# Kernel tuning notes

Hardware: AMD Instinct MI355X
Metric: run time of the kernel (lower is better)

## Reference

```python
import jax, jax.numpy as jnp
import numpy as np

B, S, H, NH = 2, 2048, 1024, 16
HD = H // NH  # head dim = 64


def setup_inputs() -> dict:
    key = jax.random.key(0)
    k_in, k_q, k_kv, k_o = jax.random.split(key, 4)
    scale = 0.02
    return {
        "inputs": jax.random.normal(k_in, (B, S, H), dtype=jnp.float32),
        "Wq": jax.random.normal(k_q, (H, H), dtype=jnp.float32) * scale,
        "bq": jnp.zeros((H,), dtype=jnp.float32),
        "Wkv": jax.random.normal(k_kv, (H, 2 * H), dtype=jnp.float32) * scale,
        "bkv": jnp.zeros((2 * H,), dtype=jnp.float32),
        "Wo": jax.random.normal(k_o, (H, H), dtype=jnp.float32) * scale,
        "bo": jnp.zeros((H,), dtype=jnp.float32),
    }


def reference(inputs, Wq, bq, Wkv, bkv, Wo, bo):
    b, s, h = inputs.shape
    q = inputs @ Wq + bq                      # [B,S,H]
    kv = inputs @ Wkv + bkv                   # [B,S,2H]
    k, v = kv[..., :h], kv[..., h:]           # each [B,S,H]
    q = q.reshape(b, s, NH, HD)
    k = k.reshape(b, s, NH, HD)
    v = v.reshape(b, s, NH, HD)
    inv_sqrt_d = jnp.asarray(1.0 / np.sqrt(HD), dtype=inputs.dtype)
    scores = jnp.einsum("bqhd,bkhd->bhqk", q, k) * inv_sqrt_d  # [B,NH,S,S]
    probs = jax.nn.softmax(scores, axis=-1)
    attended = jnp.einsum("bhqk,bkhd->bqhd", probs, v)         # [B,S,NH,HD]
    attended = attended.reshape(b, s, h)
    return attended @ Wo + bo
```

## Files before the change

### kernel.cpp

```cpp
#include <hip/hip_runtime.h>
#include <cstdint>

typedef __bf16 bf16;
typedef __attribute__((ext_vector_type(8))) __bf16 bf16x8;
typedef __attribute__((ext_vector_type(4))) __bf16 bf16v4;
typedef __attribute__((ext_vector_type(4))) float f32x4;
typedef __attribute__((ext_vector_type(16))) float f32x16;

#define MFMA16(a, b, c) __builtin_amdgcn_mfma_f32_16x16x32_bf16((a), (b), (c), 0, 0, 0)
#define MFMA32(a, b, c) __builtin_amdgcn_mfma_f32_32x32x16_bf16((a), (b), (c), 0, 0, 0)

#define BATCH 2
#define SLEN 2048
#define HDIM 1024
#define NHEAD 16
#define HEADD 64
#define MROWS (BATCH * SLEN)

#define CEXP 0.1803368801f

typedef __attribute__((address_space(3))) void lds_void;
typedef const __attribute__((address_space(1))) void glb_void;
__device__ __forceinline__ void load_lds16(const bf16* g, bf16* l) {
    __builtin_amdgcn_global_load_lds((glb_void*)g, (lds_void*)l, 16, 0, 0);
}

__global__ __launch_bounds__(256) void prep_kernel(const float* __restrict__ X,
                                                   const float* __restrict__ Wq,
                                                   const float* __restrict__ Wkv,
                                                   const float* __restrict__ Wo,
                                                   const float* __restrict__ bq,
                                                   const float* __restrict__ bkv,
                                                   bf16* __restrict__ Xbf,
                                                   bf16* __restrict__ WqkvT,
                                                   bf16* __restrict__ WoT,
                                                   float* __restrict__ bqkv) {
    const int blk = blockIdx.x;
    const int tid = threadIdx.x;
    if (blk < 4096) {
        int i = (blk * 256 + tid) * 4;
        float4 v = *(const float4*)&X[i];
        bf16v4 o;
        o[0] = (bf16)v.x; o[1] = (bf16)v.y; o[2] = (bf16)v.z; o[3] = (bf16)v.w;
        *(bf16v4*)&Xbf[i] = o;
        return;
    }
    if (blk < 8192) {
        const float* in; bf16* out; int C, id;
        if (blk < 5120)      { in = Wq;  out = WqkvT;                C = 1024; id = blk - 4096; }
        else if (blk < 7168) { in = Wkv; out = WqkvT + 1024 * 1024;  C = 2048; id = blk - 5120; }
        else                 { in = Wo;  out = WoT;                  C = 1024; id = blk - 7168; }
        const int R = 1024;
        const int nbx = C / 32;
        const int j0 = (id % nbx) * 32, i0 = (id / nbx) * 32;
        const int tx = tid & 31, ty = tid >> 5;
        __shared__ float t[32][33];
        for (int r = ty; r < 32; r += 8)
            t[r][tx] = in[(size_t)(i0 + r) * C + j0 + tx];
        __syncthreads();
        for (int r = ty; r < 32; r += 8)
            out[(size_t)(j0 + r) * R + i0 + tx] = (bf16)t[tx][r];
        return;
    }
    int i = (blk - 8192) * 256 + tid;
    if (i < 3072) bqkv[i] = (i < 1024) ? bq[i] : bkv[i - 1024];
}

template <int BM, int BN, int EPI>
__global__ __launch_bounds__(256) void gemm2_kernel(const bf16* __restrict__ A,
                                                    const bf16* __restrict__ BT,
                                                    const float* __restrict__ bias,
                                                    bf16* __restrict__ oQ,
                                                    bf16* __restrict__ oK,
                                                    bf16* __restrict__ oVT,
                                                    float* __restrict__ oF, int K) {
    constexpr int WM = BM / 2, WN = BN / 2;
    constexpr int MT = WM / 16, NT = WN / 16;

    const int tid = threadIdx.x;
    const int lane = tid & 63, wid = tid >> 6;
    const int l15 = lane & 15, quad = lane >> 4;
    const int wm = (wid >> 1) * WM, wn = (wid & 1) * WN;
    const int m0 = blockIdx.y * BM, n0 = blockIdx.x * BN;

    __shared__ bf16 As[BM * 32];
    __shared__ bf16 Bs[BN * 32];

    f32x4 acc[MT][NT] = {};

    const bf16* Ag = A + (size_t)m0 * K;
    const bf16* Bg = BT + (size_t)n0 * K;
    const int arow = lane >> 2, acol = (lane & 3) * 8;

    for (int k0 = 0; k0 < K; k0 += 32) {
#pragma unroll
        for (int t = 0; t < BM / 64; ++t) {
            int tt = t * 4 + wid;
            load_lds16(Ag + (size_t)(tt * 16 + arow) * K + k0 + acol, &As[tt * 512]);
        }
#pragma unroll
        for (int t = 0; t < BN / 64; ++t) {
            int tt = t * 4 + wid;
            load_lds16(Bg + (size_t)(tt * 16 + arow) * K + k0 + acol, &Bs[tt * 512]);
        }
        __syncthreads();

        bf16x8 af[MT], bfr[NT];
#pragma unroll
        for (int i = 0; i < MT; ++i)
            af[i] = *(const bf16x8*)&As[(wm + i * 16 + l15) * 32 + quad * 8];
#pragma unroll
        for (int j = 0; j < NT; ++j)
            bfr[j] = *(const bf16x8*)&Bs[(wn + j * 16 + l15) * 32 + quad * 8];
#pragma unroll
        for (int i = 0; i < MT; ++i)
#pragma unroll
            for (int j = 0; j < NT; ++j)
                acc[i][j] = MFMA16(af[i], bfr[j], acc[i][j]);
        __syncthreads();
    }

#pragma unroll
    for (int i = 0; i < MT; ++i) {
#pragma unroll
        for (int j = 0; j < NT; ++j) {
            const int mb = m0 + wm + i * 16 + quad * 4;
            const int n = n0 + wn + j * 16 + l15;
            const float bv = bias[n];
            if (EPI == 2) {
                float* o = oF + (size_t)mb * 1024 + n;
#pragma unroll
                for (int r = 0; r < 4; ++r) o[(size_t)r * 1024] = acc[i][j][r] + bv;
            } else if (n0 < 1024) {
#pragma unroll
                for (int r = 0; r < 4; ++r)
                    oQ[(size_t)(mb + r) * 1024 + n] = (bf16)((acc[i][j][r] + bv) * CEXP);
            } else if (n0 < 2048) {
#pragma unroll
                for (int r = 0; r < 4; ++r)
                    oK[(size_t)(mb + r) * 1024 + (n - 1024)] = (bf16)(acc[i][j][r] + bv);
            } else {
                const int hd = n - 2048;
                const int bb = mb >> 11, ss = mb & 2047;
                bf16v4 pk;
#pragma unroll
                for (int r = 0; r < 4; ++r) pk[r] = (bf16)(acc[i][j][r] + bv);
                *(bf16v4*)&oVT[((size_t)(bb << 10) + hd) * 2048 + ss] = pk;
            }
        }
    }
}

__global__ __launch_bounds__(256) void attn6_kernel(const bf16* __restrict__ Q,
                                                    const bf16* __restrict__ K,
                                                    const bf16* __restrict__ VT,
                                                    bf16* __restrict__ O) {
    const int bid = blockIdx.x;
    const int xcd = bid & 7, j = bid >> 3;
    const int bh = xcd * 4 + (j >> 4);
    const int q0 = (j & 15) * 128;
    const int b = bh >> 4, head = bh & 15;
    const int tid = threadIdx.x;
    const int lane = tid & 63, wid = tid >> 6;
    const int l31 = lane & 31, hh = lane >> 5;

    __shared__ bf16 Ks[128 * 64];
    __shared__ bf16 VTs[64 * 128];
    __shared__ bf16 Ps[4][32 * 72];

    const int qw = q0 + wid * 32;
    bf16x8 qf[4];
#pragma unroll
    for (int kd = 0; kd < 4; ++kd)
        qf[kd] = *(const bf16x8*)&Q[(size_t)(b * SLEN + qw + l31) * HDIM +
                                    head * 64 + kd * 16 + hh * 8];

    f32x16 o_acc[2] = {};
    float l_lane = 0.f;

    const bf16* Kg = K + (size_t)b * SLEN * HDIM + head * 64;
    const bf16* Vg = VT + (size_t)bh * 64 * SLEN;

    const int r8 = lane >> 3, p8 = lane & 7;
    const int r16 = lane >> 4, p16 = lane & 15;

    for (int kt = 0; kt < 16; ++kt) {
        const int k0 = kt * 128;
#pragma unroll
        for (int pass = 0; pass < 4; ++pass) {
            const int rbk = pass * 32 + wid * 8;
            load_lds16(Kg + (size_t)(k0 + rbk + r8) * HDIM + ((p8 ^ ((rbk + r8) & 7)) * 8),
                       &Ks[rbk * 64]);
            const int rbv = pass * 16 + wid * 4;
            load_lds16(Vg + (size_t)(rbv + r16) * SLEN + k0 + ((p16 ^ ((rbv + r16) & 15)) * 8),
                       &VTs[rbv * 128]);
        }
        __syncthreads();

#pragma unroll
        for (int h = 0; h < 2; ++h) {
            f32x16 sacc[2] = {};
#pragma unroll
            for (int kd = 0; kd < 4; ++kd)
#pragma unroll
                for (int m = 0; m < 2; ++m) {
                    const int key = (h * 2 + m) * 32 + l31;
                    const int c = (kd * 2 + hh) ^ (key & 7);
                    bf16x8 kf = *(const bf16x8*)&Ks[key * 64 + c * 8];
                    sacc[m] = MFMA32(kf, qf[kd], sacc[m]);
                }

#pragma unroll
            for (int m = 0; m < 2; ++m)
#pragma unroll
                for (int g = 0; g < 4; ++g) {
                    bf16v4 pk;
#pragma unroll
                    for (int r = 0; r < 4; ++r) {
                        float p = __builtin_amdgcn_exp2f(sacc[m][g * 4 + r]);
                        l_lane += p;
                        pk[r] = (bf16)p;
                    }
                    *(bf16v4*)&Ps[wid][l31 * 72 + m * 32 + g * 8 + 4 * hh] = pk;
                }

#pragma unroll
            for (int kstep = 0; kstep < 4; ++kstep) {
                bf16x8 pf = *(const bf16x8*)&Ps[wid][l31 * 72 + kstep * 16 + hh * 8];
#pragma unroll
                for (int dt = 0; dt < 2; ++dt) {
                    const int d = dt * 32 + l31;
                    const int cc = ((h * 4 + kstep) * 2 + hh) ^ (d & 15);
                    bf16x8 vf = *(const bf16x8*)&VTs[d * 128 + cc * 8];
                    o_acc[dt] = MFMA32(vf, pf, o_acc[dt]);
                }
            }
        }
        __syncthreads();
    }

    const float l_full = l_lane + __shfl_xor(l_lane, 32, 64);
    const float inv = 1.f / l_full;
    bf16* orow = O + (size_t)(b * SLEN + qw + l31) * HDIM + head * 64;
#pragma unroll
    for (int mt = 0; mt < 2; ++mt)
#pragma unroll
        for (int g = 0; g < 4; ++g) {
            bf16v4 pk;
#pragma unroll
            for (int r = 0; r < 4; ++r) pk[r] = (bf16)(o_acc[mt][g * 4 + r] * inv);
            *(bf16v4*)&orow[mt * 32 + g * 8 + 4 * hh] = pk;
        }
}

extern "C" void kernel_launch(void* const* d_in, const int* in_sizes, int n_in,
                              void* d_out, int out_size, void* d_ws, size_t ws_size,
                              hipStream_t stream) {
    const float* X   = (const float*)d_in[0];
    const float* Wq  = (const float*)d_in[1];
    const float* bq  = (const float*)d_in[2];
    const float* Wkv = (const float*)d_in[3];
    const float* bkv = (const float*)d_in[4];
    const float* Wo  = (const float*)d_in[5];
    const float* bo  = (const float*)d_in[6];
    float* out = (float*)d_out;

    char* ws = (char*)d_ws;
    bf16* Xbf   = (bf16*)(ws);
    bf16* WqkvT = (bf16*)(ws + (8ull << 20));
    bf16* WoT   = (bf16*)(ws + (14ull << 20));
    float* bqkv = (float*)(ws + (16ull << 20));
    bf16* Qbf   = (bf16*)(ws + (17ull << 20));
    bf16* Kbf   = (bf16*)(ws + (25ull << 20));
    bf16* VTbf  = (bf16*)(ws + (33ull << 20));
    bf16* Abf   = (bf16*)(ws + (41ull << 20));

    prep_kernel<<<8204, 256, 0, stream>>>(X, Wq, Wkv, Wo, bq, bkv, Xbf, WqkvT, WoT, bqkv);

    gemm2_kernel<128, 128, 1><<<dim3(3072 / 128, MROWS / 128), 256, 0, stream>>>(
        Xbf, WqkvT, bqkv, Qbf, Kbf, VTbf, nullptr, 1024);

    attn6_kernel<<<512, 256, 0, stream>>>(Qbf, Kbf, VTbf, Abf);

    gemm2_kernel<128, 64, 2><<<dim3(1024 / 64, MROWS / 128), 256, 0, stream>>>(
        Abf, WoT, bo, nullptr, nullptr, nullptr, out, 1024);
}
```

Measured before the change: 200.0 us.

## Double-buffer K/V tiles in attention and pass P via permlane swaps

The attention kernel now keeps two LDS buffers for K and V^T and prefetches the next tile with async global-to-LDS loads while the current one is computed, using explicit vmcnt waits and raw barriers instead of full syncthreads. The probability tile no longer goes through LDS. Exp results are packed into registers and rearranged into the MFMA B-operand layout with v_permlane32_swap. This aims to hide global load latency and remove the per-wave LDS write and read of P, at the cost of doubled K/V LDS footprint and reliance on a gfx950-specific permlane instruction and hand-tuned waitcnt counts.

```diff
diff --git a/kernel.cpp b/kernel.cpp
--- a/kernel.cpp
+++ b/kernel.cpp
@@ -4,8 +4,10 @@
 typedef __bf16 bf16;
 typedef __attribute__((ext_vector_type(8))) __bf16 bf16x8;
 typedef __attribute__((ext_vector_type(4))) __bf16 bf16v4;
+typedef __attribute__((ext_vector_type(2))) __bf16 bf16x2;
 typedef __attribute__((ext_vector_type(4))) float f32x4;
 typedef __attribute__((ext_vector_type(16))) float f32x16;
+typedef __attribute__((ext_vector_type(4))) unsigned u32x4;
 
 #define MFMA16(a, b, c) __builtin_amdgcn_mfma_f32_16x16x32_bf16((a), (b), (c), 0, 0, 0)
 #define MFMA32(a, b, c) __builtin_amdgcn_mfma_f32_32x32x16_bf16((a), (b), (c), 0, 0, 0)
@@ -23,6 +25,15 @@
 typedef const __attribute__((address_space(1))) void glb_void;
 __device__ __forceinline__ void load_lds16(const bf16* g, bf16* l) {
     __builtin_amdgcn_global_load_lds((glb_void*)g, (lds_void*)l, 16, 0, 0);
+}
+
+__device__ __forceinline__ void plswap(unsigned& a, unsigned& b) {
+#if __has_builtin(__builtin_amdgcn_permlane32_swap)
+    auto r = __builtin_amdgcn_permlane32_swap(a, b, false, false);
+    a = r[0]; b = r[1];
+#else
+    asm volatile("v_permlane32_swap_b32 %0, %1" : "+v"(a), "+v"(b));
+#endif
 }
 
 __global__ __launch_bounds__(256) void prep_kernel(const float* __restrict__ X,
@@ -151,7 +162,7 @@
     }
 }
 
-__global__ __launch_bounds__(256) void attn6_kernel(const bf16* __restrict__ Q,
+__global__ __launch_bounds__(256) void attn7_kernel(const bf16* __restrict__ Q,
                                                     const bf16* __restrict__ K,
                                                     const bf16* __restrict__ VT,
                                                     bf16* __restrict__ O) {
@@ -164,9 +175,8 @@
     const int lane = tid & 63, wid = tid >> 6;
     const int l31 = lane & 31, hh = lane >> 5;
 
-    __shared__ bf16 Ks[128 * 64];
-    __shared__ bf16 VTs[64 * 128];
-    __shared__ bf16 Ps[4][32 * 72];
+    __shared__ bf16 Ks[2][128 * 64];
+    __shared__ bf16 VTs[2][64 * 128];
 
     const int qw = q0 + wid * 32;
     bf16x8 qf[4];
@@ -184,18 +194,37 @@
     const int r8 = lane >> 3, p8 = lane & 7;
     const int r16 = lane >> 4, p16 = lane & 15;
 
+#pragma unroll
+    for (int pass = 0; pass < 4; ++pass) {
+        const int rbk = pass * 32 + wid * 8;
+        load_lds16(Kg + (size_t)(rbk + r8) * HDIM + ((p8 ^ ((rbk + r8) & 7)) * 8),
+                   &Ks[0][rbk * 64]);
+        const int rbv = pass * 16 + wid * 4;
+        load_lds16(Vg + (size_t)(rbv + r16) * SLEN + ((p16 ^ ((rbv + r16) & 15)) * 8),
+                   &VTs[0][rbv * 128]);
+    }
+
     for (int kt = 0; kt < 16; ++kt) {
-        const int k0 = kt * 128;
-#pragma unroll
-        for (int pass = 0; pass < 4; ++pass) {
-            const int rbk = pass * 32 + wid * 8;
-            load_lds16(Kg + (size_t)(k0 + rbk + r8) * HDIM + ((p8 ^ ((rbk + r8) & 7)) * 8),
-                       &Ks[rbk * 64]);
-            const int rbv = pass * 16 + wid * 4;
-            load_lds16(Vg + (size_t)(rbv + r16) * SLEN + k0 + ((p16 ^ ((rbv + r16) & 15)) * 8),
-                       &VTs[rbv * 128]);
-        }
-        __syncthreads();
+        const int cur = kt & 1;
+        if (kt < 15) {
+            const int k0 = (kt + 1) * 128;
+#pragma unroll
+            for (int pass = 0; pass < 4; ++pass) {
+                const int rbk = pass * 32 + wid * 8;
+                load_lds16(Kg + (size_t)(k0 + rbk + r8) * HDIM + ((p8 ^ ((rbk + r8) & 7)) * 8),
+                           &Ks[cur ^ 1][rbk * 64]);
+                const int rbv = pass * 16 + wid * 4;
+                load_lds16(Vg + (size_t)(rbv + r16) * SLEN + k0 + ((p16 ^ ((rbv + r16) & 15)) * 8),
+                           &VTs[cur ^ 1][rbv * 128]);
+            }
+            asm volatile("s_waitcnt vmcnt(8)" ::: "memory");
+        } else {
+            asm volatile("s_waitcnt vmcnt(0)" ::: "memory");
+        }
+        __builtin_amdgcn_s_barrier();
+
+        const bf16* Kc = &Ks[cur][0];
+        const bf16* Vc = &VTs[cur][0];
 
 #pragma unroll
         for (int h = 0; h < 2; ++h) {
@@ -206,37 +235,48 @@
                 for (int m = 0; m < 2; ++m) {
                     const int key = (h * 2 + m) * 32 + l31;
                     const int c = (kd * 2 + hh) ^ (key & 7);
-                    bf16x8 kf = *(const bf16x8*)&Ks[key * 64 + c * 8];
+                    bf16x8 kf = *(const bf16x8*)&Kc[key * 64 + c * 8];
                     sacc[m] = MFMA32(kf, qf[kd], sacc[m]);
                 }
 
+            unsigned wA[2][4], wB[2][4];
 #pragma unroll
             for (int m = 0; m < 2; ++m)
 #pragma unroll
                 for (int g = 0; g < 4; ++g) {
-                    bf16v4 pk;
-#pragma unroll
-                    for (int r = 0; r < 4; ++r) {
-                        float p = __builtin_amdgcn_exp2f(sacc[m][g * 4 + r]);
-                        l_lane += p;
-                        pk[r] = (bf16)p;
-                    }
-                    *(bf16v4*)&Ps[wid][l31 * 72 + m * 32 + g * 8 + 4 * hh] = pk;
+                    float p0 = __builtin_amdgcn_exp2f(sacc[m][g * 4 + 0]);
+                    float p1 = __builtin_amdgcn_exp2f(sacc[m][g * 4 + 1]);
+                    float p2 = __builtin_amdgcn_exp2f(sacc[m][g * 4 + 2]);
+                    float p3 = __builtin_amdgcn_exp2f(sacc[m][g * 4 + 3]);
+                    l_lane += (p0 + p1) + (p2 + p3);
+                    bf16x2 a, c2;
+                    a[0] = (bf16)p0; a[1] = (bf16)p1;
+                    c2[0] = (bf16)p2; c2[1] = (bf16)p3;
+                    wA[m][g] = __builtin_bit_cast(unsigned, a);
+                    wB[m][g] = __builtin_bit_cast(unsigned, c2);
                 }
 
 #pragma unroll
-            for (int kstep = 0; kstep < 4; ++kstep) {
-                bf16x8 pf = *(const bf16x8*)&Ps[wid][l31 * 72 + kstep * 16 + hh * 8];
+            for (int s = 0; s < 4; ++s) {
+                const int m = s >> 1, qa = (s & 1) * 2, qb = qa + 1;
+                unsigned x0 = wA[m][qa], x2 = wA[m][qb];
+                unsigned x1 = wB[m][qa], x3 = wB[m][qb];
+                plswap(x0, x2);
+                plswap(x1, x3);
+                u32x4 fw;
+                fw[0] = x0; fw[1] = x1; fw[2] = x2; fw[3] = x3;
+                bf16x8 pf = __builtin_bit_cast(bf16x8, fw);
 #pragma unroll
                 for (int dt = 0; dt < 2; ++dt) {
                     const int d = dt * 32 + l31;
-                    const int cc = ((h * 4 + kstep) * 2 + hh) ^ (d & 15);
-                    bf16x8 vf = *(const bf16x8*)&VTs[d * 128 + cc * 8];
+                    const int cc = ((h * 4 + s) * 2 + hh) ^ (d & 15);
+                    bf16x8 vf = *(const bf16x8*)&Vc[d * 128 + cc * 8];
                     o_acc[dt] = MFMA32(vf, pf, o_acc[dt]);
                 }
             }
         }
-        __syncthreads();
+        asm volatile("" ::: "memory");
+        __builtin_amdgcn_s_barrier();
     }
 
     const float l_full = l_lane + __shfl_xor(l_lane, 32, 64);
@@ -280,7 +320,7 @@
     gemm2_kernel<128, 128, 1><<<dim3(3072 / 128, MROWS / 128), 256, 0, stream>>>(
         Xbf, WqkvT, bqkv, Qbf, Kbf, VTbf, nullptr, 1024);
 
-    attn6_kernel<<<512, 256, 0, stream>>>(Qbf, Kbf, VTbf, Abf);
+    attn7_kernel<<<512, 256, 0, stream>>>(Qbf, Kbf, VTbf, Abf);
 
     gemm2_kernel<128, 64, 2><<<dim3(1024 / 64, MROWS / 128), 256, 0, stream>>>(
         Abf, WoT, bo, nullptr, nullptr, nullptr, out, 1024);
```

Result: no change. 196.6 us (-1.7%).
